# Optimization experiments

Measured on AMD Instinct MI355X. Metric: run time of the kernel, lower is better.

The kernel has to match this reference:

```python
import jax, jax.numpy as jnp
import numpy as np

NUM_HEADS = 12
SCRA_SCALING = 10.0
EPS = 1e-12  # F.normalize default eps


def setup_inputs() -> dict:
    key = jax.random.key(0)
    ks = jax.random.split(key, 5)
    B, N, C = 2, 2048, 768
    return {
        "x": jax.random.normal(ks[0], (B, N, C), dtype=jnp.float32),
        "qkv_w": jax.random.normal(ks[1], (3 * C, C), dtype=jnp.float32) * 0.02,
        "qkv_b": jax.random.normal(ks[2], (3 * C,), dtype=jnp.float32) * 0.02,
        "proj_w": jax.random.normal(ks[3], (C, C), dtype=jnp.float32) * 0.02,
        "proj_b": jax.random.normal(ks[4], (C,), dtype=jnp.float32) * 0.02,
    }


def reference(x, qkv_w, qkv_b, proj_w, proj_b):
    B, N, C = x.shape
    H = NUM_HEADS
    D = C // H
    scale = D ** -0.5

    xt = jnp.transpose(x, (1, 0, 2))  # [N, B, C]
    qkv = xt @ qkv_w.T + qkv_b        # [N, B, 3C]
    q, k, v = jnp.split(qkv, 3, axis=-1)

    def to_bh(t):  # [N, B, C] -> [B*H, N, D]
        return jnp.transpose(t.reshape(N, B * H, D), (1, 0, 2))

    q, k, v = to_bh(q), to_bh(k), to_bh(v)

    # Stage 1: standard attention
    attn = jax.nn.softmax(jnp.einsum('bnd,bmd->bnm', q, k) * scale, axis=-1)
    out = jnp.einsum('bnm,bmd->bnd', attn, v)  # [B*H, N, D]
    out = jnp.transpose(out, (1, 0, 2)).reshape(N, B, C)
    out = out @ proj_w.T + proj_b              # first proj
    out = jnp.transpose(out.reshape(N, B * H, D), (1, 0, 2))  # [B*H, N, D]

    # Stage 2: self-correlation attention with data-dependent masking
    norm = jnp.linalg.norm(out, axis=-1, keepdims=True)
    sim_tokens = out / jnp.maximum(norm, EPS)
    sim = jnp.einsum('bnd,bmd->bnm', sim_tokens, sim_tokens) * SCRA_SCALING
    sim = jnp.where(sim < 0, -jnp.inf, sim)
    sim = jax.nn.softmax(sim, axis=-1)
    out2 = jnp.einsum('bnm,bmd->bnd', sim, v)
    out2 = jnp.transpose(out2, (1, 0, 2)).reshape(N, B, C)
    out2 = out2 @ proj_w.T + proj_b            # second proj (same weights)

    return jnp.transpose(out2, (1, 0, 2))      # [B, N, C]
```

## Files before the change

kernel.cpp:

```cpp
#include <hip/hip_runtime.h>

typedef unsigned short u16;
typedef __bf16 bf16_t;
typedef bf16_t bf16x8 __attribute__((ext_vector_type(8)));
typedef float f32x4 __attribute__((ext_vector_type(4)));

static __device__ __forceinline__ u16 f2bf(float f) {
  unsigned u = __builtin_bit_cast(unsigned, f);
  u += 0x7FFFu + ((u >> 16) & 1u);
  return (u16)(u >> 16);
}
static __device__ __forceinline__ bf16x8 ldfrag(const u16* p) {
  return __builtin_bit_cast(bf16x8, *(const uint4*)p);
}
static __device__ __forceinline__ float fexp2(float x) {
#if __has_builtin(__builtin_amdgcn_exp2f)
  return __builtin_amdgcn_exp2f(x);
#else
  return __expf(x * 0.69314718056f);
#endif
}
static __device__ __forceinline__ unsigned pack_hi16(unsigned hi, unsigned lo) {
#if __has_builtin(__builtin_amdgcn_perm)
  return __builtin_amdgcn_perm(hi, lo, 0x07060302u);
#else
  return (lo >> 16) | (hi & 0xFFFF0000u);
#endif
}
static __device__ __forceinline__ uint4 pack8_rtz(float4 a, float4 b) {
  uint4 o;
  o.x = pack_hi16(__builtin_bit_cast(unsigned, a.y), __builtin_bit_cast(unsigned, a.x));
  o.y = pack_hi16(__builtin_bit_cast(unsigned, a.w), __builtin_bit_cast(unsigned, a.z));
  o.z = pack_hi16(__builtin_bit_cast(unsigned, b.y), __builtin_bit_cast(unsigned, b.x));
  o.w = pack_hi16(__builtin_bit_cast(unsigned, b.w), __builtin_bit_cast(unsigned, b.z));
  return o;
}
static __device__ __forceinline__ int sw(int row, int chunk) {
  return (row << 6) + ((chunk ^ (row & 7)) << 3);
}

#define QWSZ 1769472
#define PWSZ 589824

__global__ __launch_bounds__(256) void convert_w(
    const float* __restrict__ qw, const float* __restrict__ pw,
    u16* __restrict__ qwb, u16* __restrict__ pwb)
{
  const int i = (blockIdx.x * 256 + threadIdx.x) * 8;
  const float* src; u16* dst; int off;
  if (i < QWSZ) { src = qw; dst = qwb; off = i; }
  else { src = pw; dst = pwb; off = i - QWSZ; }
  float4 a = *(const float4*)(src + off), b = *(const float4*)(src + off + 4);
  u16 t[8] = {f2bf(a.x), f2bf(a.y), f2bf(a.z), f2bf(a.w),
              f2bf(b.x), f2bf(b.y), f2bf(b.z), f2bf(b.w)};
  *(uint4*)(dst + off) = *(const uint4*)t;
}

template<int MODE>
__global__ __launch_bounds__(256, MODE == 0 ? 2 : 3) void gemm_nt(
    const void* __restrict__ Araw, const u16* __restrict__ W,
    const float* __restrict__ bias,
    u16* __restrict__ d0, u16* __restrict__ d1, u16* __restrict__ d2,
    float* __restrict__ df)
{
  constexpr int BM = (MODE == 0) ? 128 : 64;
  constexpr int MI = (MODE == 0) ? 4 : 2;
  constexpr int AP = BM / 32;
  __shared__ __align__(16) u16 sA[2][BM * 64];
  __shared__ __align__(16) u16 sB[2][128 * 64];
  const float* Af = (const float*)Araw;
  const u16*   Ab = (const u16*)Araw;
  const int tid = threadIdx.x;
  const int m0 = blockIdx.y * BM, n0 = blockIdx.x * 128;
  const int w = tid >> 6, lane = tid & 63, l16 = lane & 15, quad = lane >> 4;
  const int wm = (w >> 1) * (BM / 2), wn = (w & 1) * 64;

  f32x4 acc[MI][4] = {};
  const int sr = tid >> 3, ch = tid & 7, sc = ch * 8;

  #pragma unroll
  for (int p = 0; p < AP; p++) {
    const int row = sr + p * 32;
    if (MODE == 0) {
      const float* ap = Af + (size_t)(m0 + row) * 768 + sc;
      *(uint4*)(sA[0] + sw(row, ch)) =
          pack8_rtz(*(const float4*)ap, *(const float4*)(ap + 4));
    } else {
      *(uint4*)(sA[0] + sw(row, ch)) =
          *(const uint4*)(Ab + (size_t)(m0 + row) * 768 + sc);
    }
  }
  #pragma unroll
  for (int p = 0; p < 4; p++) {
    const int row = sr + p * 32;
    *(uint4*)(sB[0] + sw(row, ch)) = *(const uint4*)(W + (size_t)(n0 + row) * 768 + sc);
  }
  __syncthreads();

  for (int kt = 0; kt < 12; kt++) {
    const int buf = kt & 1;
    const bool pre = (kt + 1 < 12);
    float4 ra0[AP], ra1[AP];
    uint4 rab[AP], rb[4];
    if (pre) {
      const int kc = (kt + 1) * 64 + sc;
      #pragma unroll
      for (int p = 0; p < AP; p++) {
        if (MODE == 0) {
          const float* ap = Af + (size_t)(m0 + sr + p * 32) * 768 + kc;
          ra0[p] = *(const float4*)ap;
          ra1[p] = *(const float4*)(ap + 4);
        } else {
          rab[p] = *(const uint4*)(Ab + (size_t)(m0 + sr + p * 32) * 768 + kc);
        }
      }
      #pragma unroll
      for (int p = 0; p < 4; p++)
        rb[p] = *(const uint4*)(W + (size_t)(n0 + sr + p * 32) * 768 + kc);
    }
    #pragma unroll
    for (int ks = 0; ks < 2; ks++) {
      bf16x8 af[MI], bfv[4];
      #pragma unroll
      for (int i = 0; i < MI; i++)
        af[i] = ldfrag(sA[buf] + sw(wm + i * 16 + l16, ks * 4 + quad));
      #pragma unroll
      for (int i = 0; i < 4; i++)
        bfv[i] = ldfrag(sB[buf] + sw(wn + i * 16 + l16, ks * 4 + quad));
      #pragma unroll
      for (int mi = 0; mi < MI; mi++)
        #pragma unroll
        for (int ni = 0; ni < 4; ni++)
          acc[mi][ni] = __builtin_amdgcn_mfma_f32_16x16x32_bf16(af[mi], bfv[ni], acc[mi][ni], 0, 0, 0);
    }
    if (pre) {
      #pragma unroll
      for (int p = 0; p < AP; p++) {
        if (MODE == 0)
          *(uint4*)(sA[buf ^ 1] + sw(sr + p * 32, ch)) = pack8_rtz(ra0[p], ra1[p]);
        else
          *(uint4*)(sA[buf ^ 1] + sw(sr + p * 32, ch)) = rab[p];
      }
      #pragma unroll
      for (int p = 0; p < 4; p++)
        *(uint4*)(sB[buf ^ 1] + sw(sr + p * 32, ch)) = rb[p];
    }
    __syncthreads();
  }

  if (MODE == 0) {
    #pragma unroll
    for (int ni = 0; ni < 4; ni++) {
      const int gn = n0 + wn + ni * 16 + l16;
      const float bv = bias[gn];
      const int which = gn / 768;
      const int c = gn - which * 768, hh = c >> 6, d = c & 63;
      #pragma unroll
      for (int mi = 0; mi < 4; mi++) {
        const int gm0 = m0 + wm + mi * 16 + quad * 4;
        const int bb = gm0 >> 11, nt0 = gm0 & 2047;
        if (which == 2) {
          u16 t[4];
          #pragma unroll
          for (int r = 0; r < 4; r++) t[r] = f2bf(acc[mi][ni][r] + bv);
          *(uint2*)(d2 + (((size_t)(bb * 12 + hh)) * 64 + d) * 2048 + nt0) =
              *(const uint2*)t;
        } else {
          u16* dst = (which == 0) ? d0 : d1;
          #pragma unroll
          for (int r = 0; r < 4; r++)
            dst[(((size_t)(bb * 12 + hh)) * 2048 + nt0 + r) * 64 + d] =
                f2bf(acc[mi][ni][r] + bv);
        }
      }
    }
  } else if (MODE == 1) {
    #pragma unroll
    for (int mi = 0; mi < MI; mi++) {
      #pragma unroll
      for (int r = 0; r < 4; r++) {
        float v[4]; float ss = 0.f;
        #pragma unroll
        for (int ni = 0; ni < 4; ni++) {
          v[ni] = acc[mi][ni][r] + bias[n0 + wn + ni * 16 + l16];
          ss += v[ni] * v[ni];
        }
        #pragma unroll
        for (int off = 1; off < 16; off <<= 1) ss += __shfl_xor(ss, off);
        const float scl = 1.f / fmaxf(sqrtf(ss), 1e-12f);
        const int gm = m0 + wm + mi * 16 + quad * 4 + r;
        const int nt = gm >> 1, b = gm & 1;
        #pragma unroll
        for (int ni = 0; ni < 4; ni++) {
          const int gn = n0 + wn + ni * 16 + l16, h = gn >> 6, d = gn & 63;
          d0[(((size_t)(b * 12 + h)) * 2048 + nt) * 64 + d] = f2bf(v[ni] * scl);
        }
      }
    }
  } else {
    #pragma unroll
    for (int ni = 0; ni < 4; ni++) {
      const int gn = n0 + wn + ni * 16 + l16;
      const float bv = bias[gn];
      #pragma unroll
      for (int mi = 0; mi < MI; mi++) {
        #pragma unroll
        for (int r = 0; r < 4; r++) {
          const int gm = m0 + wm + mi * 16 + quad * 4 + r;
          const int nt = gm >> 1, b = gm & 1;
          df[((size_t)b * 2048 + nt) * 768 + gn] = acc[mi][ni][r] + bv;
        }
      }
    }
  }
}

template<int MODE>
__global__ __launch_bounds__(256, 2) void flash_attn(
    const u16* __restrict__ Qm, const u16* __restrict__ Km,
    const u16* __restrict__ VT, u16* __restrict__ Ob)
{
  constexpr int N = 2048;
  __shared__ __align__(16) u16 sU[128 * 64];
  __shared__ __align__(16) u16 sK[2][64 * 64];
  __shared__ __align__(16) u16 sVT[2][64 * 64];
  const int tid = threadIdx.x;
  const int bh = blockIdx.y, m0 = blockIdx.x * 128;
  const int b = bh / 12, h = bh % 12;
  const int w = tid >> 6, lane = tid & 63, l16 = lane & 15, quad = lane >> 4;

  constexpr float SC = (MODE == 1) ? 0.18033688011112042f
                                   : 14.426950408889634f;
  constexpr float M0 = (MODE == 1) ? 24.f : 14.6f;

  const u16* kbase = Km + (size_t)bh * N * 64;
  const u16* vbase = VT + (size_t)bh * 64 * N;
  const int qr = tid >> 1, qc = (tid & 1) * 4;
  const int sr4 = tid >> 2, c4 = tid & 3;
  {
    const u16* qp = Qm + ((size_t)bh * N + m0 + qr) * 64 + qc * 8;
    #pragma unroll
    for (int j = 0; j < 4; j++)
      *(uint4*)(sU + sw(qr, qc + j)) = *(const uint4*)(qp + j * 8);
    const u16* kp = kbase + (size_t)sr4 * 64;
    *(uint4*)(sK[0] + sw(sr4, c4))     = *(const uint4*)(kp + c4 * 8);
    *(uint4*)(sK[0] + sw(sr4, c4 + 4)) = *(const uint4*)(kp + c4 * 8 + 32);
    const u16* vp = vbase + (size_t)sr4 * N;
    *(uint4*)(sVT[0] + sw(sr4, c4))     = *(const uint4*)(vp + c4 * 8);
    *(uint4*)(sVT[0] + sw(sr4, c4 + 4)) = *(const uint4*)(vp + c4 * 8 + 32);
  }
  __syncthreads();
  bf16x8 qf[2][2];
  #pragma unroll
  for (int qg = 0; qg < 2; qg++) {
    qf[qg][0] = ldfrag(sU + sw(w * 32 + qg * 16 + l16, quad));
    qf[qg][1] = ldfrag(sU + sw(w * 32 + qg * 16 + l16, quad + 4));
  }
  asm volatile("s_waitcnt lgkmcnt(0)" ::: "memory");

  bf16x8 ones;
  #pragma unroll
  for (int i = 0; i < 8; i++) ones[i] = (bf16_t)1.0f;

  f32x4 oacc[2][4] = {};
  f32x4 lacc[2] = {};

  for (int it = 0; it < 32; it++) {
    const int buf = it & 1;
    const u16* sKb = sK[buf];
    const u16* sVb = sVT[buf];
    u16* sKn = sK[buf ^ 1];
    u16* sVn = sVT[buf ^ 1];

    uint4 pk0, pk1, pv0, pv1;
    const bool pre = (it + 1 < 32);
    if (pre) {
      const int j1 = (it + 1) * 64;
      const u16* kp = kbase + (size_t)(j1 + sr4) * 64;
      pk0 = *(const uint4*)(kp + c4 * 8);
      pk1 = *(const uint4*)(kp + c4 * 8 + 32);
      const u16* vp = vbase + (size_t)sr4 * N + j1;
      pv0 = *(const uint4*)(vp + c4 * 8);
      pv1 = *(const uint4*)(vp + c4 * 8 + 32);
    }

    f32x4 s[2][4];
    #pragma unroll
    for (int jt = 0; jt < 4; jt++) {
      bf16x8 kf0 = ldfrag(sKb + sw(jt * 16 + l16, quad));
      bf16x8 kf1 = ldfrag(sKb + sw(jt * 16 + l16, quad + 4));
      #pragma unroll
      for (int qg = 0; qg < 2; qg++) {
        f32x4 a = {};
        a = __builtin_amdgcn_mfma_f32_16x16x32_bf16(kf0, qf[qg][0], a, 0, 0, 0);
        a = __builtin_amdgcn_mfma_f32_16x16x32_bf16(kf1, qf[qg][1], a, 0, 0, 0);
        s[qg][jt] = a;
      }
    }

    #pragma unroll
    for (int qg = 0; qg < 2; qg++) {
      const int prow = w * 32 + qg * 16 + l16;
      #pragma unroll
      for (int jt = 0; jt < 4; jt++) {
        unsigned pu[4];
        #pragma unroll
        for (int r = 0; r < 4; r++) {
          const float a = s[qg][jt][r];
          float p = fexp2(fmaf(a, SC, -M0));
          if (MODE == 2 && a < 0.f) p = 0.f;
          pu[r] = __builtin_bit_cast(unsigned, p) & 0xFFFF0000u;
        }
        uint2 pkk;
        pkk.x = pack_hi16(pu[1], pu[0]);
        pkk.y = pack_hi16(pu[3], pu[2]);
        *(uint2*)(sU + sw(prow, 2 * jt + (quad >> 1)) + (quad & 1) * 4) = pkk;
      }
    }

    asm volatile("s_waitcnt lgkmcnt(0)" ::: "memory");
    bf16x8 pf[2][2];
    #pragma unroll
    for (int qg = 0; qg < 2; qg++) {
      pf[qg][0] = ldfrag(sU + sw(w * 32 + qg * 16 + l16, quad));
      pf[qg][1] = ldfrag(sU + sw(w * 32 + qg * 16 + l16, quad + 4));
    }

    if (pre) {
      *(uint4*)(sKn + sw(sr4, c4))     = pk0;
      *(uint4*)(sKn + sw(sr4, c4 + 4)) = pk1;
      *(uint4*)(sVn + sw(sr4, c4))     = pv0;
      *(uint4*)(sVn + sw(sr4, c4 + 4)) = pv1;
    }

    #pragma unroll
    for (int d4 = 0; d4 < 4; d4++) {
      bf16x8 v0 = ldfrag(sVb + sw(d4 * 16 + l16, quad));
      bf16x8 v1 = ldfrag(sVb + sw(d4 * 16 + l16, quad + 4));
      #pragma unroll
      for (int qg = 0; qg < 2; qg++) {
        oacc[qg][d4] = __builtin_amdgcn_mfma_f32_16x16x32_bf16(v0, pf[qg][0], oacc[qg][d4], 0, 0, 0);
        oacc[qg][d4] = __builtin_amdgcn_mfma_f32_16x16x32_bf16(v1, pf[qg][1], oacc[qg][d4], 0, 0, 0);
      }
    }
    #pragma unroll
    for (int qg = 0; qg < 2; qg++) {
      lacc[qg] = __builtin_amdgcn_mfma_f32_16x16x32_bf16(ones, pf[qg][0], lacc[qg], 0, 0, 0);
      lacc[qg] = __builtin_amdgcn_mfma_f32_16x16x32_bf16(ones, pf[qg][1], lacc[qg], 0, 0, 0);
    }
    __syncthreads();
  }

  #pragma unroll
  for (int qg = 0; qg < 2; qg++) {
    const int query = m0 + w * 32 + qg * 16 + l16;
    const float inv = 1.f / fmaxf(lacc[qg][0], 1e-30f);
    u16* obase = Ob + ((size_t)query * 2 + b) * 768 + h * 64;
    #pragma unroll
    for (int d4 = 0; d4 < 4; d4++) {
      u16 t[4];
      #pragma unroll
      for (int r = 0; r < 4; r++) t[r] = f2bf(oacc[qg][d4][r] * inv);
      *(uint2*)(obase + d4 * 16 + quad * 4) = *(const uint2*)t;
    }
  }
}

extern "C" void kernel_launch(void* const* d_in, const int* in_sizes, int n_in,
                              void* d_out, int out_size, void* d_ws, size_t ws_size,
                              hipStream_t stream) {
  const float* x      = (const float*)d_in[0];
  const float* qkv_w  = (const float*)d_in[1];
  const float* qkv_b  = (const float*)d_in[2];
  const float* proj_w = (const float*)d_in[3];
  const float* proj_b = (const float*)d_in[4];
  float* out = (float*)d_out;

  const size_t SZ = (size_t)24 * 2048 * 64;
  char* ws = (char*)d_ws;
  u16* vtb = (u16*)ws;
  size_t off = SZ * 2;
  u16* qwb = (u16*)(ws + off); off += (size_t)QWSZ * 2;
  u16* pwb = (u16*)(ws + off); off += (size_t)PWSZ * 2;
  u16* qb  = (u16*)(ws + off); off += SZ * 2;
  u16* kb  = (u16*)(ws + off); off += SZ * 2;
  u16* st  = kb;
  u16* o1  = (u16*)(ws + off);
  u16* o2  = o1;

  convert_w<<<1152, 256, 0, stream>>>(qkv_w, proj_w, qwb, pwb);
  gemm_nt<0><<<dim3(18, 32), 256, 0, stream>>>(x, qwb, qkv_b, qb, kb, vtb, nullptr);
  flash_attn<1><<<dim3(16, 24), 256, 0, stream>>>(qb, kb, vtb, o1);
  gemm_nt<1><<<dim3(6, 64), 256, 0, stream>>>(o1, pwb, proj_b, st, nullptr, nullptr, nullptr);
  flash_attn<2><<<dim3(16, 24), 256, 0, stream>>>(st, st, vtb, o2);
  gemm_nt<2><<<dim3(6, 64), 256, 0, stream>>>(o2, pwb, proj_b, nullptr, nullptr, nullptr, out);
}
```

Baseline: 237.9 us.

## Split attention key range across two blocks and combine partial results

Each flash attention launch now splits the 2048 keys into two halves handled by separate blocks, doubling the grid from 384 to 768 blocks to better fill the GPU's compute units. Each block writes unnormalized fp32 output and row sums to a workspace, and a new combine kernel adds the two halves, normalizes and writes bf16. This works without max tracking because the softmax uses a fixed offset. The cost is extra global traffic for the fp32 partials plus two more kernel launches. Output buffers are moved to reuse the q buffer.

Measured after the change: 240.3 us. Within noise of the previous version (+1.0%).

```diff
diff --git a/kernel.cpp b/kernel.cpp
--- a/kernel.cpp
+++ b/kernel.cpp
@@ -218,15 +218,17 @@
 template<int MODE>
 __global__ __launch_bounds__(256, 2) void flash_attn(
     const u16* __restrict__ Qm, const u16* __restrict__ Km,
-    const u16* __restrict__ VT, u16* __restrict__ Ob)
+    const u16* __restrict__ VT,
+    float* __restrict__ partN, float* __restrict__ partL)
 {
   constexpr int N = 2048;
   __shared__ __align__(16) u16 sU[128 * 64];
   __shared__ __align__(16) u16 sK[2][64 * 64];
   __shared__ __align__(16) u16 sVT[2][64 * 64];
   const int tid = threadIdx.x;
-  const int bh = blockIdx.y, m0 = blockIdx.x * 128;
-  const int b = bh / 12, h = bh % 12;
+  const int bh = blockIdx.y;
+  const int qt = blockIdx.x >> 1, half = blockIdx.x & 1;
+  const int m0 = qt * 128, j0 = half * 1024;
   const int w = tid >> 6, lane = tid & 63, l16 = lane & 15, quad = lane >> 4;
 
   constexpr float SC = (MODE == 1) ? 0.18033688011112042f
@@ -242,10 +244,10 @@
     #pragma unroll
     for (int j = 0; j < 4; j++)
       *(uint4*)(sU + sw(qr, qc + j)) = *(const uint4*)(qp + j * 8);
-    const u16* kp = kbase + (size_t)sr4 * 64;
+    const u16* kp = kbase + (size_t)(j0 + sr4) * 64;
     *(uint4*)(sK[0] + sw(sr4, c4))     = *(const uint4*)(kp + c4 * 8);
     *(uint4*)(sK[0] + sw(sr4, c4 + 4)) = *(const uint4*)(kp + c4 * 8 + 32);
-    const u16* vp = vbase + (size_t)sr4 * N;
+    const u16* vp = vbase + (size_t)sr4 * N + j0;
     *(uint4*)(sVT[0] + sw(sr4, c4))     = *(const uint4*)(vp + c4 * 8);
     *(uint4*)(sVT[0] + sw(sr4, c4 + 4)) = *(const uint4*)(vp + c4 * 8 + 32);
   }
@@ -265,7 +267,7 @@
   f32x4 oacc[2][4] = {};
   f32x4 lacc[2] = {};
 
-  for (int it = 0; it < 32; it++) {
+  for (int it = 0; it < 16; it++) {
     const int buf = it & 1;
     const u16* sKb = sK[buf];
     const u16* sVb = sVT[buf];
@@ -273,9 +275,9 @@
     u16* sVn = sVT[buf ^ 1];
 
     uint4 pk0, pk1, pv0, pv1;
-    const bool pre = (it + 1 < 32);
+    const bool pre = (it + 1 < 16);
     if (pre) {
-      const int j1 = (it + 1) * 64;
+      const int j1 = j0 + (it + 1) * 64;
       const u16* kp = kbase + (size_t)(j1 + sr4) * 64;
       pk0 = *(const uint4*)(kp + c4 * 8);
       pk1 = *(const uint4*)(kp + c4 * 8 + 32);
@@ -351,16 +353,45 @@
     __syncthreads();
   }
 
+  const int blk = bh * 32 + blockIdx.x;
+  float* pN = partN + (size_t)blk * 8192 + tid * 32;
   #pragma unroll
   for (int qg = 0; qg < 2; qg++) {
-    const int query = m0 + w * 32 + qg * 16 + l16;
-    const float inv = 1.f / fmaxf(lacc[qg][0], 1e-30f);
+    #pragma unroll
+    for (int d4 = 0; d4 < 4; d4++)
+      *(f32x4*)(pN + qg * 16 + d4 * 4) = oacc[qg][d4];
+    if (quad == 0)
+      partL[blk * 128 + w * 32 + qg * 16 + l16] = lacc[qg][0];
+  }
+}
+
+__global__ __launch_bounds__(256) void combine_flash(
+    const float* __restrict__ partN, const float* __restrict__ partL,
+    u16* __restrict__ Ob)
+{
+  const int pair = blockIdx.x;
+  const int bh = pair >> 4, qt = pair & 15;
+  const int b = bh / 12, h = bh % 12;
+  const int m0 = qt * 128;
+  const int tid = threadIdx.x;
+  const int w = tid >> 6, lane = tid & 63, l16 = lane & 15, quad = lane >> 4;
+  const int blk0 = bh * 32 + qt * 2, blk1 = blk0 + 1;
+  const float* n0 = partN + (size_t)blk0 * 8192 + tid * 32;
+  const float* n1 = partN + (size_t)blk1 * 8192 + tid * 32;
+  #pragma unroll
+  for (int qg = 0; qg < 2; qg++) {
+    const int qrow = w * 32 + qg * 16 + l16;
+    const float l0 = partL[blk0 * 128 + qrow];
+    const float l1 = partL[blk1 * 128 + qrow];
+    const float inv = 1.f / fmaxf(l0 + l1, 1e-30f);
+    const int query = m0 + qrow;
     u16* obase = Ob + ((size_t)query * 2 + b) * 768 + h * 64;
     #pragma unroll
     for (int d4 = 0; d4 < 4; d4++) {
-      u16 t[4];
-      #pragma unroll
-      for (int r = 0; r < 4; r++) t[r] = f2bf(oacc[qg][d4][r] * inv);
+      float4 a = *(const float4*)(n0 + qg * 16 + d4 * 4);
+      float4 c = *(const float4*)(n1 + qg * 16 + d4 * 4);
+      u16 t[4] = {f2bf((a.x + c.x) * inv), f2bf((a.y + c.y) * inv),
+                  f2bf((a.z + c.z) * inv), f2bf((a.w + c.w) * inv)};
       *(uint2*)(obase + d4 * 16 + quad * 4) = *(const uint2*)t;
     }
   }
@@ -384,14 +415,18 @@
   u16* pwb = (u16*)(ws + off); off += (size_t)PWSZ * 2;
   u16* qb  = (u16*)(ws + off); off += SZ * 2;
   u16* kb  = (u16*)(ws + off); off += SZ * 2;
-  u16* st  = kb;
-  u16* o1  = (u16*)(ws + off);
-  u16* o2  = o1;
+  float* partN = (float*)(ws + off); off += (size_t)768 * 8192 * 4;
+  float* partL = (float*)(ws + off); off += (size_t)768 * 128 * 4;
+  u16* o1 = qb;
+  u16* o2 = qb;
+  u16* st = kb;
 
   convert_w<<<1152, 256, 0, stream>>>(qkv_w, proj_w, qwb, pwb);
   gemm_nt<0><<<dim3(18, 32), 256, 0, stream>>>(x, qwb, qkv_b, qb, kb, vtb, nullptr);
-  flash_attn<1><<<dim3(16, 24), 256, 0, stream>>>(qb, kb, vtb, o1);
+  flash_attn<1><<<dim3(32, 24), 256, 0, stream>>>(qb, kb, vtb, partN, partL);
+  combine_flash<<<384, 256, 0, stream>>>(partN, partL, o1);
   gemm_nt<1><<<dim3(6, 64), 256, 0, stream>>>(o1, pwb, proj_b, st, nullptr, nullptr, nullptr);
-  flash_attn<2><<<dim3(16, 24), 256, 0, stream>>>(st, st, vtb, o2);
+  flash_attn<2><<<dim3(32, 24), 256, 0, stream>>>(st, st, vtb, partN, partL);
+  combine_flash<<<384, 256, 0, stream>>>(partN, partL, o2);
   gemm_nt<2><<<dim3(6, 64), 256, 0, stream>>>(o2, pwb, proj_b, nullptr, nullptr, nullptr, out);
 }
```
